# Optimization experiments

Measured on AMD Instinct MI355X. Metric: run time of the kernel, lower is better.

## Reference

```python
import jax, jax.numpy as jnp
import numpy as np

B, T, F, H, L = 512, 512, 64, 128, 3


def setup_inputs() -> dict:
    key = jax.random.key(0)
    ks = jax.random.split(key, 6)
    s_in = 1.0 / np.sqrt(F)
    s_h = 1.0 / np.sqrt(H)
    return {
        "x": jax.random.normal(ks[0], (B, T, F), dtype=jnp.float32),
        "Wx0": jax.random.normal(ks[1], (F, 3 * H), dtype=jnp.float32) * s_in,
        "Wx_rest": jax.random.normal(ks[2], (L - 1, H, 3 * H), dtype=jnp.float32) * s_h,
        "Wh": jax.random.normal(ks[3], (L, H, 3 * H), dtype=jnp.float32) * s_h,
        "b": jnp.zeros((L, 3 * H), dtype=jnp.float32),
        "Wd": jax.random.normal(ks[4], (H, H), dtype=jnp.float32) * s_h,
        "bd": jnp.zeros((H,), dtype=jnp.float32),
    }


def _gru_layer(x_seq, Wx, Wh_l, b_l):
    """x_seq: [T, B, Din] -> [T, B, H]. Classic GRU (reset_after=False)."""
    # Precompute input projections for all timesteps in one GEMM: [T, B, 3H]
    gx = jnp.einsum("tbd,dg->tbg", x_seq, Wx) + b_l

    def step(h, gx_t):
        gh = h @ Wh_l                      # [B, 3H]
        xz, xr, xn = jnp.split(gx_t, 3, axis=-1)
        hz, hr, hn = jnp.split(gh, 3, axis=-1)
        z = jax.nn.sigmoid(xz + hz)
        r = jax.nn.sigmoid(xr + hr)
        n = jnp.tanh(xn + r * hn)
        h_new = z * h + (1.0 - z) * n
        return h_new, h_new

    h0 = jnp.zeros((x_seq.shape[1], Wh_l.shape[0]), dtype=x_seq.dtype)
    _, hs = jax.lax.scan(step, h0, gx)
    return hs                              # [T, B, H]


def reference(x, Wx0, Wx_rest, Wh, b, Wd, bd):
    h = jnp.swapaxes(x, 0, 1)              # [T, B, F] time-major for scan
    h = _gru_layer(h, Wx0, Wh[0], b[0])
    for l in range(1, L):                  # small fixed layer loop
        h = _gru_layer(h, Wx_rest[l - 1], Wh[l], b[l])
    h = jnp.swapaxes(h, 0, 1)              # [B, T, H]
    return jax.nn.sigmoid(jnp.einsum("bth,hk->btk", h, Wd) + bd)
```

## Files before the change

### kernel.cpp

```cpp
#include <hip/hip_runtime.h>

namespace {

constexpr int Bb = 512, Tt = 512, Ff = 64, Hh = 128, Gg = 384;
constexpr int CH = 64, NCH = Tt / CH;
constexpr float SZ = -1.44269504f;
constexpr float SN =  2.88539008f;

using short8  = __attribute__((ext_vector_type(8))) short;
using short4v = __attribute__((ext_vector_type(4))) short;
using f32x4   = __attribute__((ext_vector_type(4))) float;

__device__ __forceinline__ short f2bf(float f) {
  unsigned u = __float_as_uint(f);
  u += 0x7FFFu + ((u >> 16) & 1u);
  return (short)(u >> 16);
}
__device__ __forceinline__ float bf2f(short s) {
  return __uint_as_float(((unsigned)(unsigned short)s) << 16);
}

__global__ __launch_bounds__(512, 4) void prep(const float* __restrict__ Wx0,
                                               const float* __restrict__ Wxr,
                                               const float* __restrict__ Wh,
                                               const float* __restrict__ Wd,
                                               char* __restrict__ WhF,
                                               char* __restrict__ WxF,
                                               char* __restrict__ WdF) {
  const int id = blockIdx.x * 512 + threadIdx.x;
  const int lane = id & 63, lr = lane & 15, lk = lane >> 4;
  const int q = id >> 6;
  const float* src; int col, ldn, row0; char* dst; float sc;
  if (q < 288) {
    const int l = q / 96, rem = q % 96, w = rem / 12, f = rem % 12;
    const int g = f >> 2, ks = f & 3;
    src = Wh + (size_t)l * Hh * Gg; ldn = Gg;
    col = g * 128 + w * 16 + lr; row0 = ks * 32 + lk * 8;
    dst = WhF + (size_t)(q * 64 + lane) * 16;
    sc = (g < 2) ? SZ : SN;
  } else if (q < 528) {
    int p = q - 288; int base;
    if (p < 48)       { src = Wx0; base = 0; }
    else if (p < 144) { src = Wxr; base = 48; p -= 48; }
    else              { src = Wxr + (size_t)Hh * Gg; base = 144; p -= 144; }
    int ct, ks;
    if (base == 0) { ct = p >> 1; ks = p & 1; } else { ct = p >> 2; ks = p & 3; }
    ldn = Gg; col = ct * 16 + lr; row0 = ks * 32 + lk * 8;
    dst = WxF + (size_t)((base + p) * 64 + lane) * 16;
    sc = (ct < 16) ? SZ : SN;
  } else {
    const int p = q - 528;
    const int ct = p >> 2, ks = p & 3;
    src = Wd; ldn = Hh; col = ct * 16 + lr; row0 = ks * 32 + lk * 8;
    dst = WdF + (size_t)(p * 64 + lane) * 16;
    sc = SZ;
  }
  short8 v;
#pragma unroll
  for (int j = 0; j < 8; ++j) v[j] = f2bf(src[(size_t)(row0 + j) * ldn + col] * sc);
  *(short8*)dst = v;
}

template <int KS>
__device__ void gemm_phase(const void* __restrict__ src, int t0,
                           const char* __restrict__ wxf,
                           const float* __restrict__ bias,
                           char* __restrict__ gx,
                           int rb, int w, int lane, int lr, int lk) {
  short8 bw[3][KS];
  float bs[3];
#pragma unroll
  for (int c = 0; c < 3; ++c) {
    const int ct = w * 3 + c;
    bs[c] = bias[ct * 16 + lr] * (ct < 16 ? SZ : SN);
#pragma unroll
    for (int ks = 0; ks < KS; ++ks)
      bw[c][ks] = *(const short8*)(wxf + (size_t)((ct * KS + ks) * 64 + lane) * 16);
  }
#pragma unroll 2
  for (int t = 0; t < CH; ++t) {
    short8 af[KS];
    if constexpr (KS == 2) {
      const float* xr = (const float*)src;
#pragma unroll
      for (int ks = 0; ks < 2; ++ks) {
        const float* p = xr + ((size_t)(rb * 16 + lr) * Tt + t0 + t) * Ff + ks * 32 + lk * 8;
        f32x4 u0 = *(const f32x4*)p, u1 = *(const f32x4*)(p + 4);
        short8 v;
#pragma unroll
        for (int j = 0; j < 4; ++j) { v[j] = f2bf(u0[j]); v[4 + j] = f2bf(u1[j]); }
        af[ks] = v;
      }
    } else {
      const char* hr = (const char*)src;
#pragma unroll
      for (int ks = 0; ks < 4; ++ks)
        af[ks] = *(const short8*)(hr + ((size_t)t * 512 + rb * 16 + lr) * 256 +
                                  ((ks * 64 + lk * 16) ^ ((lr & 7) << 4)));
    }
#pragma unroll
    for (int c = 0; c < 3; ++c) {
      f32x4 acc = {0.f, 0.f, 0.f, 0.f};
#pragma unroll
      for (int ks = 0; ks < KS; ++ks)
        acc = __builtin_amdgcn_mfma_f32_16x16x32_bf16(af[ks], bw[c][ks], acc, 0, 0, 0);
      const int ct = w * 3 + c;
      short4v o;
#pragma unroll
      for (int i = 0; i < 4; ++i) o[i] = f2bf(acc[i] + bs[c]);
      *(short4v*)(gx + (size_t)((t * 32 + rb) * 8 + (ct & 7)) * 1536 + lane * 24 + (ct >> 3) * 8) = o;
    }
  }
}

__device__ void scan_phase(const char* __restrict__ gx,
                           const char* __restrict__ whf,
                           short* __restrict__ hstream,
                           float* __restrict__ state, int t0, int dense,
                           const char* __restrict__ wdf,
                           const float* __restrict__ bdp,
                           float* __restrict__ out,
                           int rb, char* hb, float* ob) {
  const int tid = threadIdx.x;
  const int w = tid >> 6, lane = tid & 63, lr = lane & 15, lk = lane >> 4;
  const int col = w * 16 + lr;

  short8 bwh[3][4];
#pragma unroll
  for (int g = 0; g < 3; ++g)
#pragma unroll
    for (int ks = 0; ks < 4; ++ks)
      bwh[g][ks] = *(const short8*)(whf + (size_t)((w * 12 + g * 4 + ks) * 64 + lane) * 16);

  short8 bwd[4]; float bdv = 0.f;
  if (dense) {
#pragma unroll
    for (int ks = 0; ks < 4; ++ks)
      bwd[ks] = *(const short8*)(wdf + (size_t)((w * 4 + ks) * 64 + lane) * 16);
    bdv = bdp[col] * SZ;
  }

  int hoffs[4];
#pragma unroll
  for (int i = 0; i < 4; ++i) {
    const int row = lk * 4 + i;
    hoffs[i] = row * 256 + ((col * 2) ^ ((row & 7) << 4));
  }

  float hreg[4];
  if (t0 == 0) {
#pragma unroll
    for (int i = 0; i < 4; ++i) hreg[i] = 0.f;
    short* hz = (short*)hb;
    for (int i = tid; i < 2048; i += 512) hz[i] = 0;
  } else {
    f32x4 s = *(const f32x4*)(state + (size_t)(rb * 512 + tid) * 4);
#pragma unroll
    for (int i = 0; i < 4; ++i) {
      hreg[i] = s[i];
      *(short*)(hb + hoffs[i]) = f2bf(s[i]);
    }
  }

  const char* gp = gx + (size_t)(rb * 8 + w) * 1536 + lane * 24;
  short4v pf0[3], pf1[3], pf2[3], pf3[3];
#pragma unroll
  for (int j = 0; j < 3; ++j) pf0[j] = *(const short4v*)(gp + j * 8);
#pragma unroll
  for (int j = 0; j < 3; ++j) pf1[j] = *(const short4v*)(gp + 393216 + j * 8);
  __syncthreads();

  auto STEP = [&](int t, short4v (&use)[3], short4v (&fill)[3]) {
    const int pp = t & 1;
    char* const hsrc = hb + pp * 4096;
    char* const hdst = hb + (1 - pp) * 4096;

    short8 ah[4];
#pragma unroll
    for (int ks = 0; ks < 4; ++ks)
      ah[ks] = *(const short8*)(hsrc + lr * 256 + ((ks * 64 + lk * 16) ^ ((lr & 7) << 4)));

    f32x4 aZ = {0.f, 0.f, 0.f, 0.f}, aR = aZ, aHn = aZ;
#pragma unroll
    for (int ks = 0; ks < 4; ++ks) {
      aZ  = __builtin_amdgcn_mfma_f32_16x16x32_bf16(ah[ks], bwh[0][ks], aZ, 0, 0, 0);
      aR  = __builtin_amdgcn_mfma_f32_16x16x32_bf16(ah[ks], bwh[1][ks], aR, 0, 0, 0);
      aHn = __builtin_amdgcn_mfma_f32_16x16x32_bf16(ah[ks], bwh[2][ks], aHn, 0, 0, 0);
    }
    if (t + 2 < CH) {
      const char* p = gp + (size_t)(t + 2) * 393216;
      fill[0] = *(const short4v*)p;
      fill[1] = *(const short4v*)(p + 8);
      fill[2] = *(const short4v*)(p + 16);
    }
    const int tg = t0 + t;
    if (dense && tg > 0) {
      f32x4 aD = {0.f, 0.f, 0.f, 0.f};
#pragma unroll
      for (int ks = 0; ks < 4; ++ks)
        aD = __builtin_amdgcn_mfma_f32_16x16x32_bf16(ah[ks], bwd[ks], aD, 0, 0, 0);
#pragma unroll
      for (int i = 0; i < 4; ++i)
        ob[pp * 2048 + (lk * 4 + i) * 128 + col] =
            __builtin_amdgcn_rcpf(1.f + __builtin_amdgcn_exp2f(aD[i] + bdv));
    }

    float hn4[4];
#pragma unroll
    for (int i = 0; i < 4; ++i) {
      const float gz = bf2f(use[0][i]);
      const float gr = bf2f(use[1][i]);
      const float gn = bf2f(use[2][i]);
      const float z  = __builtin_amdgcn_rcpf(1.f + __builtin_amdgcn_exp2f(aZ[i] + gz));
      const float rr = __builtin_amdgcn_rcpf(1.f + __builtin_amdgcn_exp2f(aR[i] + gr));
      const float eu = __builtin_amdgcn_exp2f(__builtin_fmaf(rr, aHn[i], gn));
      const float nn = __builtin_fmaf(-2.f, __builtin_amdgcn_rcpf(1.f + eu), 1.f);
      const float h  = __builtin_fmaf(z, hreg[i] - nn, nn);
      hn4[i] = h; hreg[i] = h;
    }
    unsigned p01, p23;
    asm("v_cvt_pk_bf16_f32 %0, %1, %2" : "=v"(p01) : "v"(hn4[0]), "v"(hn4[1]));
    asm("v_cvt_pk_bf16_f32 %0, %1, %2" : "=v"(p23) : "v"(hn4[2]), "v"(hn4[3]));
    *(short*)(hdst + hoffs[0]) = (short)(p01 & 0xffffu);
    *(short*)(hdst + hoffs[1]) = (short)(p01 >> 16);
    *(short*)(hdst + hoffs[2]) = (short)(p23 & 0xffffu);
    *(short*)(hdst + hoffs[3]) = (short)(p23 >> 16);

    __builtin_amdgcn_sched_barrier(0);
    asm volatile("s_waitcnt lgkmcnt(0)");
    __builtin_amdgcn_s_barrier();
    __builtin_amdgcn_sched_barrier(0);

    if (dense) {
      if (tg > 0) {
        f32x4 v = *(const f32x4*)(ob + pp * 2048 + tid * 4);
        *(f32x4*)(out + ((size_t)(rb * 16 + (tid >> 5)) * Tt + (tg - 1)) * Hh + (tid & 31) * 4) = v;
      }
    } else {
      short4v hv = *(const short4v*)(hdst + tid * 8);
      *(short4v*)(hstream + ((size_t)t * 512 + rb * 16 + (tid >> 5)) * 128 + (tid & 31) * 4) = hv;
    }
  };

  for (int tb = 0; tb < CH; tb += 4) {
    STEP(tb + 0, pf0, pf2);
    STEP(tb + 1, pf1, pf3);
    STEP(tb + 2, pf2, pf0);
    STEP(tb + 3, pf3, pf1);
  }

  {
    f32x4 sv;
#pragma unroll
    for (int i = 0; i < 4; ++i) sv[i] = hreg[i];
    *(f32x4*)(state + (size_t)(rb * 512 + tid) * 4) = sv;
  }

  if (dense && t0 + CH == Tt) {
    short8 ah[4];
#pragma unroll
    for (int ks = 0; ks < 4; ++ks)
      ah[ks] = *(const short8*)(hb + lr * 256 + ((ks * 64 + lk * 16) ^ ((lr & 7) << 4)));
    f32x4 aD = {0.f, 0.f, 0.f, 0.f};
#pragma unroll
    for (int ks = 0; ks < 4; ++ks)
      aD = __builtin_amdgcn_mfma_f32_16x16x32_bf16(ah[ks], bwd[ks], aD, 0, 0, 0);
#pragma unroll
    for (int i = 0; i < 4; ++i)
      out[((size_t)(rb * 16 + lk * 4 + i) * Tt + (Tt - 1)) * Hh + col] =
          __builtin_amdgcn_rcpf(1.f + __builtin_amdgcn_exp2f(aD[i] + bdv));
  }
}

struct LArgs {
  const void* src; const char* wxf; const char* whf; const float* bias;
  char* gx; short* hstream; float* state; int t0; int ksx; int dense;
};

__global__ __launch_bounds__(512, 1) void fused(LArgs a0, LArgs a1, LArgs a2,
                                                const char* __restrict__ wdf,
                                                const float* __restrict__ bd,
                                                float* __restrict__ out) {
  __shared__ char  hb[8192];
  __shared__ float ob[4096];
  const int g = blockIdx.x >> 5;
  const int rb = blockIdx.x & 31;
  LArgs a = (g == 0) ? a0 : (g == 1 ? a1 : a2);
  const int tid = threadIdx.x;
  const int w = tid >> 6, lane = tid & 63, lr = lane & 15, lk = lane >> 4;

  if (a.ksx == 2) gemm_phase<2>(a.src, a.t0, a.wxf, a.bias, a.gx, rb, w, lane, lr, lk);
  else            gemm_phase<4>(a.src, a.t0, a.wxf, a.bias, a.gx, rb, w, lane, lr, lk);

  __builtin_amdgcn_sched_barrier(0);
  asm volatile("s_waitcnt vmcnt(0)");
  __builtin_amdgcn_s_barrier();
  __builtin_amdgcn_sched_barrier(0);

  scan_phase(a.gx, a.whf, a.hstream, a.state, a.t0, a.dense, wdf, bd, out, rb, hb, ob);
}

}

extern "C" void kernel_launch(void* const* d_in, const int* in_sizes, int n_in,
                              void* d_out, int out_size, void* d_ws, size_t ws_size,
                              hipStream_t stream) {
  const float* x   = (const float*)d_in[0];
  const float* Wx0 = (const float*)d_in[1];
  const float* Wxr = (const float*)d_in[2];
  const float* Wh  = (const float*)d_in[3];
  const float* b   = (const float*)d_in[4];
  const float* Wd  = (const float*)d_in[5];
  const float* bd  = (const float*)d_in[6];
  float* out = (float*)d_out;

  char* ws = (char*)d_ws;
  char*  WhF    = ws;
  char*  WxF    = ws + 294912;
  char*  WdF    = ws + 540672;
  float* state0 = (float*)(ws + 573440);
  char*  gx0    = ws + 1441792;
  char*  gx1    = gx0 + 25165824;
  char*  gx2    = gx1 + 25165824;
  short* hc     = (short*)(ws + 76939264);

  prep<<<70, 512, 0, stream>>>(Wx0, Wxr, Wh, Wd, WhF, WxF, WdF);

  const size_t WXOFF[3] = {0, 49152, 147456};
  for (int r = 0; r < NCH + 2; ++r) {
    LArgs la[3]; int n = 0;
    for (int l = 0; l < 3; ++l) {
      const int k = r - l;
      if (k < 0 || k >= NCH) continue;
      LArgs& A = la[n++];
      A.src = (l == 0) ? (const void*)x
                       : (const void*)(hc + (size_t)((l - 1) * 2 + (k & 1)) * 4194304);
      A.wxf = WxF + WXOFF[l];
      A.whf = WhF + (size_t)l * 98304;
      A.bias = b + l * Gg;
      A.gx = (l == 0) ? gx0 : (l == 1 ? gx1 : gx2);
      A.hstream = (l < 2) ? hc + (size_t)(l * 2 + (k & 1)) * 4194304 : nullptr;
      A.state = state0 + l * 65536;
      A.t0 = k * CH;
      A.ksx = (l == 0) ? 2 : 4;
      A.dense = (l == 2) ? 1 : 0;
    }
    for (int i = n; i < 3; ++i) la[i] = la[0];
    fused<<<n * 32, 512, 0, stream>>>(la[0], la[1], la[2], WdF, bd, out);
  }
}
```

Measured before the change: 1.193 ms.

## Pair two scan teams per workgroup with staggered MFMA and gate phases

Each workgroup now holds two 512-thread teams that each own an independent 16-row batch slice. The recurrent step is split into an MFMA phase and a gate/writeback phase, and the teams are offset so one does matrix work while the other does transcendental gate math, with MFMA priority raised via s_setprio. The aim is to overlap matrix-core and vector-ALU latency on the serial critical path of the recurrence. In exchange there are twice as many block-wide barriers per step, and the launch is halved to 1024-thread blocks with doubled shared memory, which changes how blocks map onto CUs.

New measurement: 2.355 ms. +97.3%, slower.

```diff
diff --git a/kernel.cpp b/kernel.cpp
--- a/kernel.cpp
+++ b/kernel.cpp
@@ -19,6 +19,14 @@
 __device__ __forceinline__ float bf2f(short s) {
   return __uint_as_float(((unsigned)(unsigned short)s) << 16);
 }
+
+#define PBAR()                                   \
+  do {                                           \
+    __builtin_amdgcn_sched_barrier(0);           \
+    asm volatile("s_waitcnt lgkmcnt(0)");        \
+    __builtin_amdgcn_s_barrier();                \
+    __builtin_amdgcn_sched_barrier(0);           \
+  } while (0)
 
 __global__ __launch_bounds__(512, 4) void prep(const float* __restrict__ Wx0,
                                                const float* __restrict__ Wxr,
@@ -113,16 +121,15 @@
   }
 }
 
-__device__ void scan_phase(const char* __restrict__ gx,
-                           const char* __restrict__ whf,
-                           short* __restrict__ hstream,
-                           float* __restrict__ state, int t0, int dense,
-                           const char* __restrict__ wdf,
-                           const float* __restrict__ bdp,
-                           float* __restrict__ out,
-                           int rb, char* hb, float* ob) {
-  const int tid = threadIdx.x;
-  const int w = tid >> 6, lane = tid & 63, lr = lane & 15, lk = lane >> 4;
+__device__ void scan_team(const char* __restrict__ gx,
+                          const char* __restrict__ whf,
+                          short* __restrict__ hstream,
+                          float* __restrict__ state, int t0, int dense,
+                          const char* __restrict__ wdf,
+                          const float* __restrict__ bdp,
+                          float* __restrict__ out,
+                          int rb, int team, int ltid, char* hb, float* ob) {
+  const int w = ltid >> 6, lane = ltid & 63, lr = lane & 15, lk = lane >> 4;
   const int col = w * 16 + lr;
 
   short8 bwh[3][4];
@@ -152,9 +159,9 @@
 #pragma unroll
     for (int i = 0; i < 4; ++i) hreg[i] = 0.f;
     short* hz = (short*)hb;
-    for (int i = tid; i < 2048; i += 512) hz[i] = 0;
+    for (int i = ltid; i < 2048; i += 512) hz[i] = 0;
   } else {
-    f32x4 s = *(const f32x4*)(state + (size_t)(rb * 512 + tid) * 4);
+    f32x4 s = *(const f32x4*)(state + (size_t)(rb * 512 + ltid) * 4);
 #pragma unroll
     for (int i = 0; i < 4; ++i) {
       hreg[i] = s[i];
@@ -163,39 +170,33 @@
   }
 
   const char* gp = gx + (size_t)(rb * 8 + w) * 1536 + lane * 24;
-  short4v pf0[3], pf1[3], pf2[3], pf3[3];
-#pragma unroll
-  for (int j = 0; j < 3; ++j) pf0[j] = *(const short4v*)(gp + j * 8);
-#pragma unroll
-  for (int j = 0; j < 3; ++j) pf1[j] = *(const short4v*)(gp + 393216 + j * 8);
-  __syncthreads();
-
-  auto STEP = [&](int t, short4v (&use)[3], short4v (&fill)[3]) {
+  f32x4 aZ = {0.f, 0.f, 0.f, 0.f}, aR = aZ, aHn = aZ;
+
+  auto R_M = [&](int t) {
     const int pp = t & 1;
-    char* const hsrc = hb + pp * 4096;
-    char* const hdst = hb + (1 - pp) * 4096;
-
+    const char* hsrc = hb + pp * 4096;
+    if (!dense && t > 0) {
+      short4v hv = *(const short4v*)(hsrc + ltid * 8);
+      *(short4v*)(hstream + ((size_t)(t - 1) * 512 + rb * 16 + (ltid >> 5)) * 128 +
+                  (ltid & 31) * 4) = hv;
+    }
     short8 ah[4];
 #pragma unroll
     for (int ks = 0; ks < 4; ++ks)
       ah[ks] = *(const short8*)(hsrc + lr * 256 + ((ks * 64 + lk * 16) ^ ((lr & 7) << 4)));
-
-    f32x4 aZ = {0.f, 0.f, 0.f, 0.f}, aR = aZ, aHn = aZ;
+    const f32x4 z4 = {0.f, 0.f, 0.f, 0.f};
+    aZ = z4; aR = z4; aHn = z4;
+    __builtin_amdgcn_s_setprio(1);
 #pragma unroll
     for (int ks = 0; ks < 4; ++ks) {
       aZ  = __builtin_amdgcn_mfma_f32_16x16x32_bf16(ah[ks], bwh[0][ks], aZ, 0, 0, 0);
       aR  = __builtin_amdgcn_mfma_f32_16x16x32_bf16(ah[ks], bwh[1][ks], aR, 0, 0, 0);
       aHn = __builtin_amdgcn_mfma_f32_16x16x32_bf16(ah[ks], bwh[2][ks], aHn, 0, 0, 0);
     }
-    if (t + 2 < CH) {
-      const char* p = gp + (size_t)(t + 2) * 393216;
-      fill[0] = *(const short4v*)p;
-      fill[1] = *(const short4v*)(p + 8);
-      fill[2] = *(const short4v*)(p + 16);
-    }
+    __builtin_amdgcn_s_setprio(0);
     const int tg = t0 + t;
     if (dense && tg > 0) {
-      f32x4 aD = {0.f, 0.f, 0.f, 0.f};
+      f32x4 aD = z4;
 #pragma unroll
       for (int ks = 0; ks < 4; ++ks)
         aD = __builtin_amdgcn_mfma_f32_16x16x32_bf16(ah[ks], bwd[ks], aD, 0, 0, 0);
@@ -204,16 +205,24 @@
         ob[pp * 2048 + (lk * 4 + i) * 128 + col] =
             __builtin_amdgcn_rcpf(1.f + __builtin_amdgcn_exp2f(aD[i] + bdv));
     }
-
+  };
+
+  auto G_W = [&](int t, short4v (&pf)[3]) {
+    const int pp = t & 1;
+    char* const hdst = hb + (1 - pp) * 4096;
+    const short4v g0 = pf[0], g1 = pf[1], g2 = pf[2];
+    if (t + 2 < CH) {
+      const char* p = gp + (size_t)(t + 2) * 393216;
+      pf[0] = *(const short4v*)p;
+      pf[1] = *(const short4v*)(p + 8);
+      pf[2] = *(const short4v*)(p + 16);
+    }
     float hn4[4];
 #pragma unroll
     for (int i = 0; i < 4; ++i) {
-      const float gz = bf2f(use[0][i]);
-      const float gr = bf2f(use[1][i]);
-      const float gn = bf2f(use[2][i]);
-      const float z  = __builtin_amdgcn_rcpf(1.f + __builtin_amdgcn_exp2f(aZ[i] + gz));
-      const float rr = __builtin_amdgcn_rcpf(1.f + __builtin_amdgcn_exp2f(aR[i] + gr));
-      const float eu = __builtin_amdgcn_exp2f(__builtin_fmaf(rr, aHn[i], gn));
+      const float z  = __builtin_amdgcn_rcpf(1.f + __builtin_amdgcn_exp2f(aZ[i] + bf2f(g0[i])));
+      const float rr = __builtin_amdgcn_rcpf(1.f + __builtin_amdgcn_exp2f(aR[i] + bf2f(g1[i])));
+      const float eu = __builtin_amdgcn_exp2f(__builtin_fmaf(rr, aHn[i], bf2f(g2[i])));
       const float nn = __builtin_fmaf(-2.f, __builtin_amdgcn_rcpf(1.f + eu), 1.f);
       const float h  = __builtin_fmaf(z, hreg[i] - nn, nn);
       hn4[i] = h; hreg[i] = h;
@@ -225,38 +234,45 @@
     *(short*)(hdst + hoffs[1]) = (short)(p01 >> 16);
     *(short*)(hdst + hoffs[2]) = (short)(p23 & 0xffffu);
     *(short*)(hdst + hoffs[3]) = (short)(p23 >> 16);
-
-    __builtin_amdgcn_sched_barrier(0);
-    asm volatile("s_waitcnt lgkmcnt(0)");
-    __builtin_amdgcn_s_barrier();
-    __builtin_amdgcn_sched_barrier(0);
-
-    if (dense) {
-      if (tg > 0) {
-        f32x4 v = *(const f32x4*)(ob + pp * 2048 + tid * 4);
-        *(f32x4*)(out + ((size_t)(rb * 16 + (tid >> 5)) * Tt + (tg - 1)) * Hh + (tid & 31) * 4) = v;
-      }
-    } else {
-      short4v hv = *(const short4v*)(hdst + tid * 8);
-      *(short4v*)(hstream + ((size_t)t * 512 + rb * 16 + (tid >> 5)) * 128 + (tid & 31) * 4) = hv;
+    const int tg = t0 + t;
+    if (dense && tg > 0) {
+      f32x4 v = *(const f32x4*)(ob + pp * 2048 + ltid * 4);
+      *(f32x4*)(out + ((size_t)(rb * 16 + (ltid >> 5)) * Tt + (tg - 1)) * Hh +
+                (ltid & 31) * 4) = v;
     }
   };
 
-  for (int tb = 0; tb < CH; tb += 4) {
-    STEP(tb + 0, pf0, pf2);
-    STEP(tb + 1, pf1, pf3);
-    STEP(tb + 2, pf2, pf0);
-    STEP(tb + 3, pf3, pf1);
-  }
+  short4v pfA[3], pfB[3];
+#pragma unroll
+  for (int j = 0; j < 3; ++j) pfA[j] = *(const short4v*)(gp + j * 8);
+#pragma unroll
+  for (int j = 0; j < 3; ++j) pfB[j] = *(const short4v*)(gp + 393216 + j * 8);
+  __syncthreads();
+
+  for (int tb = 0; tb < CH; tb += 2) {
+    if (team == 0) R_M(tb); else if (tb > 0) G_W(tb - 1, pfB);
+    PBAR();
+    if (team == 0) G_W(tb, pfA); else R_M(tb);
+    PBAR();
+    if (team == 0) R_M(tb + 1); else G_W(tb, pfA);
+    PBAR();
+    if (team == 0) G_W(tb + 1, pfB); else R_M(tb + 1);
+    PBAR();
+  }
+  if (team == 1) G_W(CH - 1, pfB);
+  PBAR();
 
   {
     f32x4 sv;
 #pragma unroll
     for (int i = 0; i < 4; ++i) sv[i] = hreg[i];
-    *(f32x4*)(state + (size_t)(rb * 512 + tid) * 4) = sv;
-  }
-
-  if (dense && t0 + CH == Tt) {
+    *(f32x4*)(state + (size_t)(rb * 512 + ltid) * 4) = sv;
+  }
+  if (!dense) {
+    short4v hv = *(const short4v*)(hb + ltid * 8);
+    *(short4v*)(hstream + ((size_t)(CH - 1) * 512 + rb * 16 + (ltid >> 5)) * 128 +
+                (ltid & 31) * 4) = hv;
+  } else if (t0 + CH == Tt) {
     short8 ah[4];
 #pragma unroll
     for (int ks = 0; ks < 4; ++ks)
@@ -277,17 +293,19 @@
   char* gx; short* hstream; float* state; int t0; int ksx; int dense;
 };
 
-__global__ __launch_bounds__(512, 1) void fused(LArgs a0, LArgs a1, LArgs a2,
-                                                const char* __restrict__ wdf,
-                                                const float* __restrict__ bd,
-                                                float* __restrict__ out) {
-  __shared__ char  hb[8192];
-  __shared__ float ob[4096];
-  const int g = blockIdx.x >> 5;
-  const int rb = blockIdx.x & 31;
+__global__ __launch_bounds__(1024, 1) void fused(LArgs a0, LArgs a1, LArgs a2,
+                                                 const char* __restrict__ wdf,
+                                                 const float* __restrict__ bd,
+                                                 float* __restrict__ out) {
+  __shared__ char  hb[2][8192];
+  __shared__ float ob[2][4096];
+  const int g = blockIdx.x >> 4;
   LArgs a = (g == 0) ? a0 : (g == 1 ? a1 : a2);
   const int tid = threadIdx.x;
-  const int w = tid >> 6, lane = tid & 63, lr = lane & 15, lk = lane >> 4;
+  const int team = tid >> 9;
+  const int ltid = tid & 511;
+  const int rb = (blockIdx.x & 15) * 2 + team;
+  const int w = ltid >> 6, lane = ltid & 63, lr = lane & 15, lk = lane >> 4;
 
   if (a.ksx == 2) gemm_phase<2>(a.src, a.t0, a.wxf, a.bias, a.gx, rb, w, lane, lr, lk);
   else            gemm_phase<4>(a.src, a.t0, a.wxf, a.bias, a.gx, rb, w, lane, lr, lk);
@@ -297,7 +315,8 @@
   __builtin_amdgcn_s_barrier();
   __builtin_amdgcn_sched_barrier(0);
 
-  scan_phase(a.gx, a.whf, a.hstream, a.state, a.t0, a.dense, wdf, bd, out, rb, hb, ob);
+  scan_team(a.gx, a.whf, a.hstream, a.state, a.t0, a.dense, wdf, bd, out,
+            rb, team, ltid, hb[team], ob[team]);
 }
 
 }
@@ -346,6 +365,6 @@
       A.dense = (l == 2) ? 1 : 0;
     }
     for (int i = n; i < 3; ++i) la[i] = la[0];
-    fused<<<n * 32, 512, 0, stream>>>(la[0], la[1], la[2], WdF, bd, out);
-  }
-}
+    fused<<<n * 16, 1024, 0, stream>>>(la[0], la[1], la[2], WdF, bd, out);
+  }
+}
```

## Replace per-step workgroup barrier with LDS atomic counter spin-wait

Applied to the files above, without the earlier changes.

Each recurrent step now ends with one atomic increment per wave on an LDS counter instead of s_barrier. Before reading the shared hidden state, a wave spins until all eight waves have finished the previous step, so waves can drift apart instead of lockstepping. The dense output is written straight to global memory, dropping the LDS staging buffer and its readback. The hstream copy now happens after the wait on the source buffer. Risks are LDS polling contention, a bounded spin that could silently fall through, and less coalesced output stores.

Result: slower. 1.259 ms (+5.5%).

```diff
diff --git a/kernel.cpp b/kernel.cpp
--- a/kernel.cpp
+++ b/kernel.cpp
@@ -120,7 +120,7 @@
                            const char* __restrict__ wdf,
                            const float* __restrict__ bdp,
                            float* __restrict__ out,
-                           int rb, char* hb, float* ob) {
+                           int rb, char* hb, int* cnt) {
   const int tid = threadIdx.x;
   const int w = tid >> 6, lane = tid & 63, lr = lane & 15, lk = lane >> 4;
   const int col = w * 16 + lr;
@@ -146,6 +146,8 @@
     const int row = lk * 4 + i;
     hoffs[i] = row * 256 + ((col * 2) ^ ((row & 7) << 4));
   }
+
+  if (tid == 0) *cnt = 0;
 
   float hreg[4];
   if (t0 == 0) {
@@ -170,10 +172,27 @@
   for (int j = 0; j < 3; ++j) pf1[j] = *(const short4v*)(gp + 393216 + j * 8);
   __syncthreads();
 
-  auto STEP = [&](int t, short4v (&use)[3], short4v (&fill)[3]) {
-    const int pp = t & 1;
-    char* const hsrc = hb + pp * 4096;
-    char* const hdst = hb + (1 - pp) * 4096;
+  auto WAIT = [&](int target) {
+    int budget = 1 << 22;
+    while (__hip_atomic_load(cnt, __ATOMIC_RELAXED, __HIP_MEMORY_SCOPE_WORKGROUP) < target &&
+           --budget) {}
+    __builtin_amdgcn_sched_barrier(0);
+  };
+
+  auto STEP = [&](int s, short4v (&use)[3], short4v (&fill)[3]) {
+    const int pin = s & 1;
+    const char* hsrc = hb + pin * 4096;
+    char* const hdst = hb + (1 - pin) * 4096;
+    const int tg = t0 + s;
+
+    if (s > 0) {
+      WAIT(8 * s);
+      if (!dense) {
+        short4v hv = *(const short4v*)(hsrc + tid * 8);
+        *(short4v*)(hstream + ((size_t)(s - 1) * 512 + rb * 16 + (tid >> 5)) * 128 +
+                    (tid & 31) * 4) = hv;
+      }
+    }
 
     short8 ah[4];
 #pragma unroll
@@ -187,13 +206,12 @@
       aR  = __builtin_amdgcn_mfma_f32_16x16x32_bf16(ah[ks], bwh[1][ks], aR, 0, 0, 0);
       aHn = __builtin_amdgcn_mfma_f32_16x16x32_bf16(ah[ks], bwh[2][ks], aHn, 0, 0, 0);
     }
-    if (t + 2 < CH) {
-      const char* p = gp + (size_t)(t + 2) * 393216;
+    if (s + 2 < CH) {
+      const char* p = gp + (size_t)(s + 2) * 393216;
       fill[0] = *(const short4v*)p;
       fill[1] = *(const short4v*)(p + 8);
       fill[2] = *(const short4v*)(p + 16);
     }
-    const int tg = t0 + t;
     if (dense && tg > 0) {
       f32x4 aD = {0.f, 0.f, 0.f, 0.f};
 #pragma unroll
@@ -201,19 +219,16 @@
         aD = __builtin_amdgcn_mfma_f32_16x16x32_bf16(ah[ks], bwd[ks], aD, 0, 0, 0);
 #pragma unroll
       for (int i = 0; i < 4; ++i)
-        ob[pp * 2048 + (lk * 4 + i) * 128 + col] =
+        out[((size_t)(rb * 16 + lk * 4 + i) * Tt + (tg - 1)) * Hh + col] =
             __builtin_amdgcn_rcpf(1.f + __builtin_amdgcn_exp2f(aD[i] + bdv));
     }
 
     float hn4[4];
 #pragma unroll
     for (int i = 0; i < 4; ++i) {
-      const float gz = bf2f(use[0][i]);
-      const float gr = bf2f(use[1][i]);
-      const float gn = bf2f(use[2][i]);
-      const float z  = __builtin_amdgcn_rcpf(1.f + __builtin_amdgcn_exp2f(aZ[i] + gz));
-      const float rr = __builtin_amdgcn_rcpf(1.f + __builtin_amdgcn_exp2f(aR[i] + gr));
-      const float eu = __builtin_amdgcn_exp2f(__builtin_fmaf(rr, aHn[i], gn));
+      const float z  = __builtin_amdgcn_rcpf(1.f + __builtin_amdgcn_exp2f(aZ[i] + bf2f(use[0][i])));
+      const float rr = __builtin_amdgcn_rcpf(1.f + __builtin_amdgcn_exp2f(aR[i] + bf2f(use[1][i])));
+      const float eu = __builtin_amdgcn_exp2f(__builtin_fmaf(rr, aHn[i], bf2f(use[2][i])));
       const float nn = __builtin_fmaf(-2.f, __builtin_amdgcn_rcpf(1.f + eu), 1.f);
       const float h  = __builtin_fmaf(z, hreg[i] - nn, nn);
       hn4[i] = h; hreg[i] = h;
@@ -228,18 +243,9 @@
 
     __builtin_amdgcn_sched_barrier(0);
     asm volatile("s_waitcnt lgkmcnt(0)");
-    __builtin_amdgcn_s_barrier();
     __builtin_amdgcn_sched_barrier(0);
-
-    if (dense) {
-      if (tg > 0) {
-        f32x4 v = *(const f32x4*)(ob + pp * 2048 + tid * 4);
-        *(f32x4*)(out + ((size_t)(rb * 16 + (tid >> 5)) * Tt + (tg - 1)) * Hh + (tid & 31) * 4) = v;
-      }
-    } else {
-      short4v hv = *(const short4v*)(hdst + tid * 8);
-      *(short4v*)(hstream + ((size_t)t * 512 + rb * 16 + (tid >> 5)) * 128 + (tid & 31) * 4) = hv;
-    }
+    if (lane == 0) atomicAdd(cnt, 1);
+    __builtin_amdgcn_sched_barrier(0);
   };
 
   for (int tb = 0; tb < CH; tb += 4) {
@@ -249,14 +255,19 @@
     STEP(tb + 3, pf3, pf1);
   }
 
+  WAIT(8 * CH);
+
   {
     f32x4 sv;
 #pragma unroll
     for (int i = 0; i < 4; ++i) sv[i] = hreg[i];
     *(f32x4*)(state + (size_t)(rb * 512 + tid) * 4) = sv;
   }
-
-  if (dense && t0 + CH == Tt) {
+  if (!dense) {
+    short4v hv = *(const short4v*)(hb + tid * 8);
+    *(short4v*)(hstream + ((size_t)(CH - 1) * 512 + rb * 16 + (tid >> 5)) * 128 +
+                (tid & 31) * 4) = hv;
+  } else if (t0 + CH == Tt) {
     short8 ah[4];
 #pragma unroll
     for (int ks = 0; ks < 4; ++ks)
@@ -281,8 +292,8 @@
                                                 const char* __restrict__ wdf,
                                                 const float* __restrict__ bd,
                                                 float* __restrict__ out) {
-  __shared__ char  hb[8192];
-  __shared__ float ob[4096];
+  __shared__ char hb[8192];
+  __shared__ int  cnt;
   const int g = blockIdx.x >> 5;
   const int rb = blockIdx.x & 31;
   LArgs a = (g == 0) ? a0 : (g == 1 ? a1 : a2);
@@ -297,7 +308,8 @@
   __builtin_amdgcn_s_barrier();
   __builtin_amdgcn_sched_barrier(0);
 
-  scan_phase(a.gx, a.whf, a.hstream, a.state, a.t0, a.dense, wdf, bd, out, rb, hb, ob);
+  scan_phase(a.gx, a.whf, a.hstream, a.state, a.t0, a.dense, wdf, bd, out,
+             rb, hb, &cnt);
 }
 
 }
```
